# Optimization experiments

Hardware: AMD Instinct MI355X
Metric: run time of the kernel (lower is better)

Reference implementation:

```python
import jax, jax.numpy as jnp
import numpy as np

N_NODES = 100000
N_EDGES = 1600000
IN_DIM = 4
HID = 64


def gcn_conv(x, src, dst, W, b, num_nodes):
    """PyG GCNConv: out = D^-1/2 (A+I) D^-1/2 (x @ W) + b, add aggregation."""
    loop = jnp.arange(num_nodes)
    src_f = jnp.concatenate([src, loop])  # [E+N]
    dst_f = jnp.concatenate([dst, loop])
    # degree from destination (col) counts, self loops included -> deg >= 1
    deg = jax.ops.segment_sum(jnp.ones_like(dst_f, dtype=x.dtype), dst_f,
                              num_segments=num_nodes)
    dinv = jax.lax.rsqrt(deg)
    norm = dinv[src_f] * dinv[dst_f]  # [E+N]
    h = x @ W  # [N, out] transform first (cheaper when out <= in is false too; matches PyG)
    msg = h[src_f] * norm[:, None]  # [E+N, out]
    out = jax.ops.segment_sum(msg, dst_f, num_segments=num_nodes)
    return out + b


def setup_inputs() -> dict:
    key = jax.random.key(0)
    ks = jax.random.split(key, 6)
    x = jax.random.normal(ks[0], (N_NODES, IN_DIM), dtype=jnp.float32)
    edge_index = jax.random.randint(ks[1], (2, N_EDGES), 0, N_NODES, dtype=jnp.int64)
    # glorot-ish scaled weights
    W1 = jax.random.normal(ks[2], (IN_DIM, HID), dtype=jnp.float32) / np.sqrt(IN_DIM)
    b1 = jnp.zeros((HID,), dtype=jnp.float32)
    W2 = jax.random.normal(ks[3], (HID, HID), dtype=jnp.float32) / np.sqrt(HID)
    b2 = jnp.zeros((HID,), dtype=jnp.float32)
    Wl = jax.random.normal(ks[4], (HID, 1), dtype=jnp.float32) / np.sqrt(HID)
    bl = jnp.zeros((1,), dtype=jnp.float32)
    return {"x": x, "edge_index": edge_index, "W1": W1, "b1": b1,
            "W2": W2, "b2": b2, "Wl": Wl, "bl": bl}


def reference(x, edge_index, W1, b1, W2, b2, Wl, bl):
    num_nodes = x.shape[0]
    src, dst = edge_index[0], edge_index[1]
    h = jax.nn.relu(gcn_conv(x, src, dst, W1, b1, num_nodes))
    h = jax.nn.relu(gcn_conv(h, src, dst, W2, b2, num_nodes))
    logits = (h @ Wl + bl).squeeze(-1)  # [N]
    return logits
```

## Files before the change

### kernel.cpp

```cpp
#include <hip/hip_runtime.h>

#define NN 100000
#define NE 1600000
#define HID 64
#define NBUK 391
#define SRCBITS 17
#define SRCMASK 0x1FFFF
#define EBLK 4096
#define GE2 ((NE + EBLK - 1) / EBLK)
#define BSTRIDE 6144

typedef __attribute__((ext_vector_type(8))) short bf16x8;
typedef __attribute__((ext_vector_type(4))) float f32x4;

__device__ __forceinline__ unsigned short f2bf(float f) {
    unsigned int x = __float_as_uint(f);
    return (unsigned short)((x + 0x7FFFu + ((x >> 16) & 1u)) >> 16);
}

__global__ void __launch_bounds__(256)
k_fill1(const int* __restrict__ ei, int* __restrict__ gcnt,
        int* __restrict__ arrival, int* __restrict__ bucketBase,
        unsigned int* __restrict__ bbuf) {
    __shared__ int s_src[EBLK];
    __shared__ int s_dst[EBLK];
    __shared__ int s_hist[NBUK];
    __shared__ int s_tmp[256];
    __shared__ int s_flag;
    __shared__ int s_last;
    int t = threadIdx.x;
    int b = blockIdx.x;

    for (int i = t; i < NBUK; i += 256) s_hist[i] = 0;
    if (t < 64) {
        unsigned long long bal = __ballot(ei[2 * t + 1] != 0);
        if (t == 0) s_flag = (bal == 0ULL) ? 1 : 0;
    }
    __syncthreads();
    int f = s_flag;
    int base = b * EBLK;
    int m = NE - base; if (m > EBLK) m = EBLK;

    if (f) {
        const int4* ps = (const int4*)ei;
        const int4* pd = (const int4*)(ei + 2 * (size_t)NE);
#pragma unroll
        for (int k = 0; k < EBLK / 512; ++k) {
            int e = base + k * 512 + t * 2;
            if (e < NE) {
                int4 vs = ps[e >> 1];
                int4 vd = pd[e >> 1];
                int l = e - base;
                s_src[l] = vs.x;     s_dst[l] = vd.x;
                s_src[l + 1] = vs.z; s_dst[l + 1] = vd.z;
                atomicAdd(&s_hist[vd.x >> 8], 1);
                atomicAdd(&s_hist[vd.z >> 8], 1);
            }
        }
    } else {
        const int4* ps = (const int4*)ei;
        const int4* pd = (const int4*)(ei + NE);
#pragma unroll
        for (int k = 0; k < EBLK / 1024; ++k) {
            int e = base + k * 1024 + t * 4;
            if (e < NE) {
                int4 vs = ps[e >> 2];
                int4 vd = pd[e >> 2];
                int l = e - base;
                s_src[l] = vs.x; s_src[l + 1] = vs.y; s_src[l + 2] = vs.z; s_src[l + 3] = vs.w;
                s_dst[l] = vd.x; s_dst[l + 1] = vd.y; s_dst[l + 2] = vd.z; s_dst[l + 3] = vd.w;
                atomicAdd(&s_hist[vd.x >> 8], 1);
                atomicAdd(&s_hist[vd.y >> 8], 1);
                atomicAdd(&s_hist[vd.z >> 8], 1);
                atomicAdd(&s_hist[vd.w >> 8], 1);
            }
        }
    }
    __syncthreads();
    for (int i = t; i < NBUK; i += 256) {
        int c = s_hist[i];
        int r = atomicAdd(&gcnt[i], c);
        s_hist[i] = i * BSTRIDE + r;
    }
    __syncthreads();
    for (int e = t; e < m; e += 256) {
        int d = s_dst[e];
        int p = atomicAdd(&s_hist[d >> 8], 1);
        bbuf[p] = ((unsigned int)(d & 255) << SRCBITS) | (unsigned int)s_src[e];
    }
    __syncthreads();
    if (t == 0) s_last = atomicAdd(arrival, 1);
    __syncthreads();
    if (s_last == GE2 - 1) {
        int i0 = 2 * t, i1 = 2 * t + 1;
        int v0 = (i0 < NBUK) ? atomicAdd(&gcnt[i0], 0) : 0;
        int v1 = (i1 < NBUK) ? atomicAdd(&gcnt[i1], 0) : 0;
        int ps2 = v0 + v1;
        s_tmp[t] = ps2; __syncthreads();
        for (int off = 1; off < 256; off <<= 1) {
            int u = (t >= off) ? s_tmp[t - off] : 0;
            __syncthreads();
            s_tmp[t] += u;
            __syncthreads();
        }
        int run = s_tmp[t] - ps2;
        if (i0 <= NBUK) bucketBase[i0] = run;
        if (i1 <= NBUK) bucketBase[i1] = run + v0;
    }
}

__global__ void k_passB(const unsigned int* __restrict__ bbuf, const int* __restrict__ gcnt,
                        const int* __restrict__ bucketBase, const float* __restrict__ x,
                        int* __restrict__ cnt, int* __restrict__ offs,
                        float* __restrict__ dinv, float* __restrict__ xs,
                        int* __restrict__ csr) {
    __shared__ int hist[256];
    __shared__ int scn[256];
    __shared__ int cur[256];
    int t = threadIdx.x;
    int b = blockIdx.x;
    int sz = gcnt[b];
    int csrbase = bucketBase[b];
    const unsigned int* buf = bbuf + (size_t)b * BSTRIDE;
    hist[t] = 0;
    __syncthreads();
    for (int e = t; e < sz; e += 256)
        atomicAdd(&hist[buf[e] >> SRCBITS], 1);
    __syncthreads();
    int deg = hist[t];
    scn[t] = deg; __syncthreads();
    for (int off = 1; off < 256; off <<= 1) {
        int u = (t >= off) ? scn[t - off] : 0;
        __syncthreads();
        scn[t] += u;
        __syncthreads();
    }
    int myoff = csrbase + scn[t] - deg;
    int node = b * 256 + t;
    if (node < NN) {
        cnt[node]  = deg;
        offs[node] = myoff;
        float d = 1.0f / sqrtf((float)(deg + 1));
        dinv[node] = d;
        float4 xv = ((const float4*)x)[node];
        float4 o; o.x = d * xv.x; o.y = d * xv.y; o.z = d * xv.z; o.w = d * xv.w;
        ((float4*)xs)[node] = o;
    }
    cur[t] = myoff;
    __syncthreads();
    for (int e = t; e < sz; e += 256) {
        unsigned int u = buf[e];
        int p = atomicAdd(&cur[u >> SRCBITS], 1);
        csr[p] = (int)(u & SRCMASK);
    }
}

__global__ void k_mm2(const float* __restrict__ xs, const int* __restrict__ cnt,
                      const int* __restrict__ offs, const int* __restrict__ csr,
                      const float* __restrict__ dinv,
                      const float* __restrict__ W1, const float* __restrict__ b1,
                      const float* __restrict__ W2, float* __restrict__ hs) {
    __shared__ unsigned short h1b[64 * 72];
    __shared__ unsigned short w2t[64 * 72];
    __shared__ float4 sPart[256];
    __shared__ float4 sAgg[64];
    __shared__ float4 sXs[64];
    __shared__ float sW1[256];
    __shared__ float sb1[64];
    __shared__ float sdv[64];
    __shared__ int scnt[64];
    __shared__ int soff[64];
    int t = threadIdx.x;
    int base = blockIdx.x * 64;
    if (t < 64) {
        int g = base + t;
        bool ok = (g < NN);
        scnt[t] = ok ? cnt[g] : 0;
        soff[t] = ok ? offs[g] : 0;
        sdv[t]  = ok ? dinv[g] : 0.f;
        sXs[t]  = ok ? ((const float4*)xs)[g] : make_float4(0.f, 0.f, 0.f, 0.f);
        sb1[t]  = b1[t];
    }
    sW1[t] = W1[t];
    for (int i = t; i < 4096; i += 256) {
        int k = i >> 6, n = i & 63;
        w2t[n * 72 + k] = f2bf(W2[i]);
    }
    if (blockIdx.x == 0 && t >= 128 && t < 192) hs[NN * 64 + (t - 128)] = 0.f;
    __syncthreads();
    {
        int node_l = t & 63, part = t >> 6;
        int n = scnt[node_l], b0 = soff[node_l];
        float4 s = make_float4(0.f, 0.f, 0.f, 0.f);
        int j = part;
        for (; j + 4 < n; j += 8) {
            int s0 = csr[b0 + j], s1 = csr[b0 + j + 4];
            float4 v0 = ((const float4*)xs)[s0];
            float4 v1 = ((const float4*)xs)[s1];
            s.x += v0.x + v1.x; s.y += v0.y + v1.y;
            s.z += v0.z + v1.z; s.w += v0.w + v1.w;
        }
        for (; j < n; j += 4) {
            int s0 = csr[b0 + j];
            float4 v = ((const float4*)xs)[s0];
            s.x += v.x; s.y += v.y; s.z += v.z; s.w += v.w;
        }
        sPart[t] = s;
    }
    __syncthreads();
    if (t < 64) {
        float4 a = sPart[t], b = sPart[t + 64], c = sPart[t + 128], d = sPart[t + 192];
        float4 xi = sXs[t];
        float dn = sdv[t];
        float4 o;
        o.x = dn * (a.x + b.x + c.x + d.x + xi.x);
        o.y = dn * (a.y + b.y + c.y + d.y + xi.y);
        o.z = dn * (a.z + b.z + c.z + d.z + xi.z);
        o.w = dn * (a.w + b.w + c.w + d.w + xi.w);
        sAgg[t] = o;
    }
    __syncthreads();
#pragma unroll
    for (int i = 0; i < 16; ++i) {
        int e = i * 256 + t;
        int nl = e >> 6, c = e & 63;
        float4 a = sAgg[nl];
        float h = fmaf(a.x, sW1[c], fmaf(a.y, sW1[64 + c],
                  fmaf(a.z, sW1[128 + c], fmaf(a.w, sW1[192 + c], sb1[c]))));
        h1b[nl * 72 + c] = f2bf(fmaxf(h, 0.f));
    }
    __syncthreads();
    int w = t >> 6, lane = t & 63, l15 = lane & 15, quad = lane >> 4;
    bf16x8 a0 = *(const bf16x8*)&h1b[(w * 16 + l15) * 72 + quad * 8];
    bf16x8 a1 = *(const bf16x8*)&h1b[(w * 16 + l15) * 72 + 32 + quad * 8];
    f32x4 acc[4];
#pragma unroll
    for (int nt = 0; nt < 4; ++nt) {
        bf16x8 bb0 = *(const bf16x8*)&w2t[(nt * 16 + l15) * 72 + quad * 8];
        bf16x8 bb1 = *(const bf16x8*)&w2t[(nt * 16 + l15) * 72 + 32 + quad * 8];
        f32x4 c = {0.f, 0.f, 0.f, 0.f};
        c = __builtin_amdgcn_mfma_f32_16x16x32_bf16(a0, bb0, c, 0, 0, 0);
        c = __builtin_amdgcn_mfma_f32_16x16x32_bf16(a1, bb1, c, 0, 0, 0);
        acc[nt] = c;
    }
#pragma unroll
    for (int nt = 0; nt < 4; ++nt) {
#pragma unroll
        for (int r = 0; r < 4; ++r) {
            int localn = w * 16 + quad * 4 + r;
            int g = base + localn;
            if (g < NN) hs[g * 64 + nt * 16 + l15] = acc[nt][r] * sdv[localn];
        }
    }
}

__global__ void k_gather_head(const float* __restrict__ hs, const int* __restrict__ offs,
                              const int* __restrict__ cnt, const int* __restrict__ csr,
                              const float* __restrict__ dinv, const float* __restrict__ b2,
                              const float* __restrict__ Wl, const float* __restrict__ bl,
                              float* __restrict__ out) {
    int t = threadIdx.x;
    int node = blockIdx.x * 4 + (t >> 6);
    int c = t & 63;
    int rg = c >> 4;
    int sl = c & 15;
    int b = offs[node], n = cnt[node];
    const float4* h4 = (const float4*)hs;
    int myidx = (c < n) ? csr[b + c] : NN;

    float4 A = make_float4(0.f, 0.f, 0.f, 0.f);
    int m = n < 64 ? n : 64;
    for (int j = 0; j < m; j += 32) {
        int s0 = __shfl(myidx, j + rg,      64);
        int s1 = __shfl(myidx, j + 4 + rg,  64);
        int s2 = __shfl(myidx, j + 8 + rg,  64);
        int s3 = __shfl(myidx, j + 12 + rg, 64);
        int s4 = __shfl(myidx, j + 16 + rg, 64);
        int s5 = __shfl(myidx, j + 20 + rg, 64);
        int s6 = __shfl(myidx, j + 24 + rg, 64);
        int s7 = __shfl(myidx, j + 28 + rg, 64);
        float4 v0 = h4[s0 * 16 + sl];
        float4 v1 = h4[s1 * 16 + sl];
        float4 v2 = h4[s2 * 16 + sl];
        float4 v3 = h4[s3 * 16 + sl];
        float4 v4 = h4[s4 * 16 + sl];
        float4 v5 = h4[s5 * 16 + sl];
        float4 v6 = h4[s6 * 16 + sl];
        float4 v7 = h4[s7 * 16 + sl];
        A.x += ((v0.x + v1.x) + (v2.x + v3.x)) + ((v4.x + v5.x) + (v6.x + v7.x));
        A.y += ((v0.y + v1.y) + (v2.y + v3.y)) + ((v4.y + v5.y) + (v6.y + v7.y));
        A.z += ((v0.z + v1.z) + (v2.z + v3.z)) + ((v4.z + v5.z) + (v6.z + v7.z));
        A.w += ((v0.w + v1.w) + (v2.w + v3.w)) + ((v4.w + v5.w) + (v6.w + v7.w));
    }
    for (int j = 64; j < n; j += 4) {
        int e = j + rg;
        int s = (e < n) ? csr[b + e] : NN;
        float4 v = h4[s * 16 + sl];
        A.x += v.x; A.y += v.y; A.z += v.z; A.w += v.w;
    }
    A.x += __shfl_xor(A.x, 16, 64); A.x += __shfl_xor(A.x, 32, 64);
    A.y += __shfl_xor(A.y, 16, 64); A.y += __shfl_xor(A.y, 32, 64);
    A.z += __shfl_xor(A.z, 16, 64); A.z += __shfl_xor(A.z, 32, 64);
    A.w += __shfl_xor(A.w, 16, 64); A.w += __shfl_xor(A.w, 32, 64);
    float4 vS = h4[node * 16 + sl];
    A.x += vS.x; A.y += vS.y; A.z += vS.z; A.w += vS.w;

    float4 bv = ((const float4*)b2)[sl];
    float4 wv = ((const float4*)Wl)[sl];
    float dn = dinv[node];
    float v = fmaxf(fmaf(dn, A.x, bv.x), 0.f) * wv.x
            + fmaxf(fmaf(dn, A.y, bv.y), 0.f) * wv.y
            + fmaxf(fmaf(dn, A.z, bv.z), 0.f) * wv.z
            + fmaxf(fmaf(dn, A.w, bv.w), 0.f) * wv.w;
    v += __shfl_xor(v, 1, 64);
    v += __shfl_xor(v, 2, 64);
    v += __shfl_xor(v, 4, 64);
    v += __shfl_xor(v, 8, 64);
    if (c == 0) out[node] = v + bl[0];
}

extern "C" void kernel_launch(void* const* d_in, const int* in_sizes, int n_in,
                              void* d_out, int out_size, void* d_ws, size_t ws_size,
                              hipStream_t stream) {
    const float* x  = (const float*)d_in[0];
    const int*   ei = (const int*)d_in[1];
    const float* W1 = (const float*)d_in[2];
    const float* b1 = (const float*)d_in[3];
    const float* W2 = (const float*)d_in[4];
    const float* b2 = (const float*)d_in[5];
    const float* Wl = (const float*)d_in[6];
    const float* bl = (const float*)d_in[7];
    float* out = (float*)d_out;

    char* w = (char*)d_ws;
    float* dinv  = (float*)w;                  w += NN * 4;
    int*   cnt   = (int*)w;                    w += NN * 4;
    int*   offs  = (int*)w;                    w += NN * 4;
    int*   csr   = (int*)w;                    w += NE * 4;
    float* xs    = (float*)w;                  w += NN * 4 * 4;
    float* hs    = (float*)w;                  w += (size_t)(NN + 1) * HID * 4;
    int*   gcnt  = (int*)w;                    w += NBUK * 4;
    int*   arrival = (int*)w;                  w += 4;
    int*   bucketBase = (int*)w;               w += (NBUK + 1) * 4;
    w = (char*)(((size_t)w + 255) & ~(size_t)255);
    unsigned int* bbuf = (unsigned int*)w;     w += (size_t)NBUK * BSTRIDE * 4;

    const int GMM = (NN + 63) / 64;

    hipMemsetAsync(gcnt, 0, (NBUK + 1) * sizeof(int), stream);
    hipLaunchKernelGGL(k_fill1, dim3(GE2),  dim3(256), 0, stream,
                       ei, gcnt, arrival, bucketBase, bbuf);
    hipLaunchKernelGGL(k_passB, dim3(NBUK), dim3(256), 0, stream,
                       bbuf, gcnt, bucketBase, x, cnt, offs, dinv, xs, csr);
    hipLaunchKernelGGL(k_mm2, dim3(GMM), dim3(256), 0, stream,
                       xs, cnt, offs, csr, dinv, W1, b1, W2, hs);
    hipLaunchKernelGGL(k_gather_head, dim3(NN / 4), dim3(256), 0, stream,
                       hs, offs, cnt, csr, dinv, b2, Wl, bl, out);
}
```

Baseline: 188.9 us.

## Store layer-2 features as bf16 and remap gather to 16 lanes per node

The intermediate hs matrix is now written as bf16 instead of fp32, which halves its footprint and the bytes moved by the random-access neighbour gather. The gather kernel is reorganised so each group of 16 lanes handles one node, with 4 nodes per wavefront. Each lane loads 8-byte chunks and walks that node's edges directly, replacing the previous shuffle-based index distribution. This cuts gather bandwidth and shuffle overhead, at the cost of bf16 rounding error in hs and possible lane divergence when the four nodes in a wavefront have different degrees.

```diff
diff --git a/kernel.cpp b/kernel.cpp
--- a/kernel.cpp
+++ b/kernel.cpp
@@ -17,6 +17,8 @@
     unsigned int x = __float_as_uint(f);
     return (unsigned short)((x + 0x7FFFu + ((x >> 16) & 1u)) >> 16);
 }
+__device__ __forceinline__ float bflo(unsigned int u) { return __uint_as_float(u << 16); }
+__device__ __forceinline__ float bfhi(unsigned int u) { return __uint_as_float(u & 0xFFFF0000u); }
 
 __global__ void __launch_bounds__(256)
 k_fill1(const int* __restrict__ ei, int* __restrict__ gcnt,
@@ -159,7 +161,7 @@
                       const int* __restrict__ offs, const int* __restrict__ csr,
                       const float* __restrict__ dinv,
                       const float* __restrict__ W1, const float* __restrict__ b1,
-                      const float* __restrict__ W2, float* __restrict__ hs) {
+                      const float* __restrict__ W2, unsigned short* __restrict__ hs) {
     __shared__ unsigned short h1b[64 * 72];
     __shared__ unsigned short w2t[64 * 72];
     __shared__ float4 sPart[256];
@@ -186,7 +188,7 @@
         int k = i >> 6, n = i & 63;
         w2t[n * 72 + k] = f2bf(W2[i]);
     }
-    if (blockIdx.x == 0 && t >= 128 && t < 192) hs[NN * 64 + (t - 128)] = 0.f;
+    if (blockIdx.x == 0 && t >= 128 && t < 192) hs[NN * 64 + (t - 128)] = 0;
     __syncthreads();
     {
         int node_l = t & 63, part = t >> 6;
@@ -249,62 +251,41 @@
         for (int r = 0; r < 4; ++r) {
             int localn = w * 16 + quad * 4 + r;
             int g = base + localn;
-            if (g < NN) hs[g * 64 + nt * 16 + l15] = acc[nt][r] * sdv[localn];
-        }
-    }
-}
-
-__global__ void k_gather_head(const float* __restrict__ hs, const int* __restrict__ offs,
+            if (g < NN) hs[g * 64 + nt * 16 + l15] = f2bf(acc[nt][r] * sdv[localn]);
+        }
+    }
+}
+
+__global__ void k_gather_head(const unsigned short* __restrict__ hs, const int* __restrict__ offs,
                               const int* __restrict__ cnt, const int* __restrict__ csr,
                               const float* __restrict__ dinv, const float* __restrict__ b2,
                               const float* __restrict__ Wl, const float* __restrict__ bl,
                               float* __restrict__ out) {
     int t = threadIdx.x;
-    int node = blockIdx.x * 4 + (t >> 6);
     int c = t & 63;
-    int rg = c >> 4;
+    int g = c >> 4;
     int sl = c & 15;
+    int node = blockIdx.x * 16 + (t >> 6) * 4 + g;
     int b = offs[node], n = cnt[node];
-    const float4* h4 = (const float4*)hs;
-    int myidx = (c < n) ? csr[b + c] : NN;
-
+    const uint2* hrow = (const uint2*)hs;
+    const int* ce = csr + b;
     float4 A = make_float4(0.f, 0.f, 0.f, 0.f);
-    int m = n < 64 ? n : 64;
-    for (int j = 0; j < m; j += 32) {
-        int s0 = __shfl(myidx, j + rg,      64);
-        int s1 = __shfl(myidx, j + 4 + rg,  64);
-        int s2 = __shfl(myidx, j + 8 + rg,  64);
-        int s3 = __shfl(myidx, j + 12 + rg, 64);
-        int s4 = __shfl(myidx, j + 16 + rg, 64);
-        int s5 = __shfl(myidx, j + 20 + rg, 64);
-        int s6 = __shfl(myidx, j + 24 + rg, 64);
-        int s7 = __shfl(myidx, j + 28 + rg, 64);
-        float4 v0 = h4[s0 * 16 + sl];
-        float4 v1 = h4[s1 * 16 + sl];
-        float4 v2 = h4[s2 * 16 + sl];
-        float4 v3 = h4[s3 * 16 + sl];
-        float4 v4 = h4[s4 * 16 + sl];
-        float4 v5 = h4[s5 * 16 + sl];
-        float4 v6 = h4[s6 * 16 + sl];
-        float4 v7 = h4[s7 * 16 + sl];
-        A.x += ((v0.x + v1.x) + (v2.x + v3.x)) + ((v4.x + v5.x) + (v6.x + v7.x));
-        A.y += ((v0.y + v1.y) + (v2.y + v3.y)) + ((v4.y + v5.y) + (v6.y + v7.y));
-        A.z += ((v0.z + v1.z) + (v2.z + v3.z)) + ((v4.z + v5.z) + (v6.z + v7.z));
-        A.w += ((v0.w + v1.w) + (v2.w + v3.w)) + ((v4.w + v5.w) + (v6.w + v7.w));
-    }
-    for (int j = 64; j < n; j += 4) {
-        int e = j + rg;
-        int s = (e < n) ? csr[b + e] : NN;
-        float4 v = h4[s * 16 + sl];
-        A.x += v.x; A.y += v.y; A.z += v.z; A.w += v.w;
-    }
-    A.x += __shfl_xor(A.x, 16, 64); A.x += __shfl_xor(A.x, 32, 64);
-    A.y += __shfl_xor(A.y, 16, 64); A.y += __shfl_xor(A.y, 32, 64);
-    A.z += __shfl_xor(A.z, 16, 64); A.z += __shfl_xor(A.z, 32, 64);
-    A.w += __shfl_xor(A.w, 16, 64); A.w += __shfl_xor(A.w, 32, 64);
-    float4 vS = h4[node * 16 + sl];
-    A.x += vS.x; A.y += vS.y; A.z += vS.z; A.w += vS.w;
-
+#define ACC2(u) do { \
+    A.x += bflo(u.x); A.y += bfhi(u.x); A.z += bflo(u.y); A.w += bfhi(u.y); } while (0)
+    for (int j = 0; j < n; j += 4) {
+        int i0 = ce[j];
+        int i1 = (j + 1 < n) ? ce[j + 1] : NN;
+        int i2 = (j + 2 < n) ? ce[j + 2] : NN;
+        int i3 = (j + 3 < n) ? ce[j + 3] : NN;
+        uint2 u0 = hrow[i0 * 16 + sl];
+        uint2 u1 = hrow[i1 * 16 + sl];
+        uint2 u2 = hrow[i2 * 16 + sl];
+        uint2 u3 = hrow[i3 * 16 + sl];
+        ACC2(u0); ACC2(u1); ACC2(u2); ACC2(u3);
+    }
+    uint2 uS = hrow[node * 16 + sl];
+    ACC2(uS);
+#undef ACC2
     float4 bv = ((const float4*)b2)[sl];
     float4 wv = ((const float4*)Wl)[sl];
     float dn = dinv[node];
@@ -316,7 +297,7 @@
     v += __shfl_xor(v, 2, 64);
     v += __shfl_xor(v, 4, 64);
     v += __shfl_xor(v, 8, 64);
-    if (c == 0) out[node] = v + bl[0];
+    if (sl == 0) out[node] = v + bl[0];
 }
 
 extern "C" void kernel_launch(void* const* d_in, const int* in_sizes, int n_in,
@@ -338,7 +319,7 @@
     int*   offs  = (int*)w;                    w += NN * 4;
     int*   csr   = (int*)w;                    w += NE * 4;
     float* xs    = (float*)w;                  w += NN * 4 * 4;
-    float* hs    = (float*)w;                  w += (size_t)(NN + 1) * HID * 4;
+    unsigned short* hs = (unsigned short*)w;   w += (size_t)(NN + 1) * HID * 2;
     int*   gcnt  = (int*)w;                    w += NBUK * 4;
     int*   arrival = (int*)w;                  w += 4;
     int*   bucketBase = (int*)w;               w += (NBUK + 1) * 4;
@@ -354,6 +335,6 @@
                        bbuf, gcnt, bucketBase, x, cnt, offs, dinv, xs, csr);
     hipLaunchKernelGGL(k_mm2, dim3(GMM), dim3(256), 0, stream,
                        xs, cnt, offs, csr, dinv, W1, b1, W2, hs);
-    hipLaunchKernelGGL(k_gather_head, dim3(NN / 4), dim3(256), 0, stream,
+    hipLaunchKernelGGL(k_gather_head, dim3(NN / 16), dim3(256), 0, stream,
                        hs, offs, cnt, csr, dinv, b2, Wl, bl, out);
 }
```

Result: faster. 172.1 us (-8.9%).
